# Kernel tuning notes

Measured on AMD Instinct MI355X. Metric: run time of the kernel, lower is better.

## Reference

```python
import jax, jax.numpy as jnp
import numpy as np

D1, D2, DK, NH = 1024, 1024, 1024, 1
B, S = 4, 2048


def setup_inputs() -> dict:
    key = jax.random.key(0)
    ks = jax.random.split(key, 12)
    scale1 = 1.0 / np.sqrt(D1)
    scale2 = 1.0 / np.sqrt(D2)
    scalek = 1.0 / np.sqrt(DK)
    return {
        "x": jax.random.normal(ks[0], (B, S, D1), dtype=jnp.float32),
        "y": jax.random.normal(ks[1], (B, S, D2), dtype=jnp.float32),
        "adj": jax.random.uniform(ks[2], (B, S, S), dtype=jnp.float32),
        "Wq": jax.random.uniform(ks[3], (D1, DK), jnp.float32, -scale1, scale1),
        "bq": jax.random.uniform(ks[4], (DK,), jnp.float32, -scale1, scale1),
        "Wk": jax.random.uniform(ks[5], (D2, DK), jnp.float32, -scale2, scale2),
        "bk": jax.random.uniform(ks[6], (DK,), jnp.float32, -scale2, scale2),
        "Wv": jax.random.uniform(ks[7], (D2, DK), jnp.float32, -scale2, scale2),
        "bv": jax.random.uniform(ks[8], (DK,), jnp.float32, -scale2, scale2),
        "Wo": jax.random.uniform(ks[9], (DK, D2), jnp.float32, -scalek, scalek),
        "bo": jax.random.uniform(ks[10], (D2,), jnp.float32, -scalek, scalek),
    }


def reference(x, y, adj, Wq, bq, Wk, bk, Wv, bv, Wo, bo):
    # Single-head (n_heads=1) cross-attention with additive adjacency bias.
    dk_head = DK // NH
    norm = 1.0 / np.sqrt(DK)
    Q = (x @ Wq + bq).reshape(NH, B, S, dk_head)   # [h,b,s,d]
    K = (y @ Wk + bk).reshape(NH, B, S, dk_head)
    V = (y @ Wv + bv).reshape(NH, B, S, dk_head)
    att = jnp.einsum('hbsd,hbtd->hbst', Q, K) * norm  # [h,b,s,t]
    att = jax.nn.softmax(att + adj, axis=-1)          # adj [b,s,t] broadcasts over h
    tmp = jnp.einsum('hbst,hbtd->hbsd', att, V).reshape(B, S, -1)  # [b,s,dk]
    out = (tmp @ Wo + bo).reshape(-1, S, D2)
    return out
```

## Files before the change

### kernel.cpp

```cpp
#include <hip/hip_runtime.h>
#include <stdint.h>

typedef unsigned short u16;
using bf16x8 = __attribute__((ext_vector_type(8))) short;
using f32x4  = __attribute__((ext_vector_type(4))) float;

#define NORM 0.03125f

enum { M_PROJ = 0, M_EXP = 1, M_PV = 2, M_OUT = 3 };

__device__ __forceinline__ u16 f2bf(float f) {
  uint32_t u = __float_as_uint(f);
  return (u16)((u + 0x7FFFu + ((u >> 16) & 1u)) >> 16);
}

__device__ __forceinline__ void gload_lds16(const void* g, void* lds) {
  __builtin_amdgcn_global_load_lds(
      (const __attribute__((address_space(1))) uint32_t*)g,
      (__attribute__((address_space(3))) uint32_t*)lds, 16, 0, 0);
}

__global__ void k_cvt(const float* __restrict__ in, u16* __restrict__ out, int n4) {
  int i = blockIdx.x * blockDim.x + threadIdx.x;
  if (i >= n4) return;
  float4 v = ((const float4*)in)[i];
  uint32_t lo = f2bf(v.x) | ((uint32_t)f2bf(v.y) << 16);
  uint32_t hi = f2bf(v.z) | ((uint32_t)f2bf(v.w) << 16);
  ((uint2*)out)[i] = make_uint2(lo, hi);
}

__global__ void k_tc(const float* __restrict__ W0, const float* __restrict__ W1,
                     const float* __restrict__ W2, const float* __restrict__ W3,
                     u16* __restrict__ dst) {
  __shared__ float t[64][65];
  const float* W = blockIdx.z == 0 ? W0 : blockIdx.z == 1 ? W1 : blockIdx.z == 2 ? W2 : W3;
  u16* WT = dst + (size_t)blockIdx.z * (1024 * 1024);
  int c0 = blockIdx.x * 64, r0 = blockIdx.y * 64;
  int c = threadIdx.x & 63, q = threadIdx.x >> 6;
  for (int r = q; r < 64; r += 4) t[r][c] = W[(size_t)(r0 + r) * 1024 + c0 + c];
  __syncthreads();
  for (int r = q; r < 64; r += 4) WT[(size_t)(c0 + r) * 1024 + r0 + c] = f2bf(t[c][r]);
}

struct GArgs {
  const u16* A; const u16* B; int lda, ldb; long long bstrideB; int K;
  const float* bias; const float* adj; float* dpart; const float* dpart_r;
  void* C; int ldc;
  const u16* A1; const u16* B1; const u16* B2;
  const float* bias1; const float* bias2; void* C1; void* C2;
};

template <int MODE>
__global__ __launch_bounds__(512, 2) void gemm3(GArgs g) {
  __shared__ __align__(16) u16 sm[73728];

  const int tid = threadIdx.x, lane = tid & 63, wid = tid >> 6;
  const int wm = wid >> 2, wn = wid & 3;
  const int m0 = blockIdx.x * 128;
  const int n0 = blockIdx.y * 256;
  const int b = m0 >> 11;

  const u16* A = g.A; const u16* B = g.B;
  const float* bias = g.bias; void* C = g.C;
  int zmode = 0;
  if constexpr (MODE == M_PROJ) {
    int z = blockIdx.z; zmode = z;
    if (z == 1) { A = g.A1; B = g.B1; bias = g.bias1; C = g.C1; }
    else if (z == 2) { A = g.A1; B = g.B2; bias = g.bias2; C = g.C2; }
  }
  const int lda = g.lda, ldb = g.ldb, K = g.K, NT = K >> 6;
  const u16* Bp = B + (size_t)b * g.bstrideB;

  f32x4 acc[4][4] = {};

  const int srow = tid >> 2;
  const int scb = (tid & 3) * 16;
  auto stageA = [&](int v, int kh, int bufb) {
    int csw = scb ^ ((srow & 8) << 2);
    gload_lds16(A + (size_t)(m0 + srow) * lda + v * 64 + kh * 32 + (csw >> 1),
                (void*)&sm[bufb + kh * 4096 + srow * 32 + (tid & 3) * 8]);
  };
  auto stageB = [&](int v, int kh, int bufb) {
#pragma unroll
    for (int j = 0; j < 2; ++j) {
      int row = j * 128 + srow;
      int csw = scb ^ ((row & 8) << 2);
      gload_lds16(Bp + (size_t)(n0 + row) * ldb + v * 64 + kh * 32 + (csw >> 1),
                  (void*)&sm[bufb + 8192 + kh * 8192 + row * 32 + (tid & 3) * 8]);
    }
  };

  stageA(0, 0, 0);     stageB(0, 0, 0);
  stageA(0, 1, 0);     stageB(0, 1, 0);
  stageA(1, 0, 24576); stageB(1, 0, 24576);
  stageA(1, 1, 24576); stageB(1, 1, 24576);

  const int cb = (lane >> 4) * 16;
  const int fr = lane & 15;
  int rd = 0;
  for (int u = 0; u < NT; ++u) {
    const int bufb = rd * 24576;
    const int stb = (rd == 0 ? 2 : rd - 1) * 24576;
    if (u + 1 < NT) asm volatile("s_waitcnt vmcnt(6)" ::: "memory");
    else            asm volatile("s_waitcnt vmcnt(0)" ::: "memory");
    __builtin_amdgcn_s_barrier();
#pragma unroll
    for (int kh = 0; kh < 2; ++kh) {
      bf16x8 af[4], bfr[4];
#pragma unroll
      for (int m = 0; m < 4; ++m) {
        int row = wm * 64 + m * 16 + fr;
        af[m] = *(const bf16x8*)__builtin_assume_aligned(
            &sm[bufb + kh * 4096 + row * 32 + ((cb ^ ((row & 8) << 2)) >> 1)], 16);
      }
#pragma unroll
      for (int n = 0; n < 4; ++n) {
        int row = wn * 64 + n * 16 + fr;
        bfr[n] = *(const bf16x8*)__builtin_assume_aligned(
            &sm[bufb + 8192 + kh * 8192 + row * 32 + ((cb ^ ((row & 8) << 2)) >> 1)], 16);
      }
      if (u + 2 < NT) {
        stageA(u + 2, kh, stb);
        stageB(u + 2, kh, stb);
      }
      __builtin_amdgcn_s_setprio(1);
#pragma unroll
      for (int m = 0; m < 4; ++m)
#pragma unroll
        for (int n = 0; n < 4; ++n)
          acc[m][n] = __builtin_amdgcn_mfma_f32_16x16x32_bf16(
              af[m], bfr[n], acc[m][n], 0, 0, 0);
      __builtin_amdgcn_s_setprio(0);
    }
    rd = (rd == 2) ? 0 : rd + 1;
  }

  const int lr = lane >> 4, lc = lane & 15;

  if constexpr (MODE == M_PROJ) {
    if (zmode < 2) {
      u16* Cc = (u16*)C;
#pragma unroll
      for (int m = 0; m < 4; ++m)
#pragma unroll
        for (int n = 0; n < 4; ++n) {
          int gcol = n0 + wn * 64 + n * 16 + lc;
          float bv = bias[gcol];
#pragma unroll
          for (int r = 0; r < 4; ++r) {
            int grow = m0 + wm * 64 + m * 16 + lr * 4 + r;
            Cc[(size_t)grow * g.ldc + gcol] = f2bf(acc[m][n][r] + bv);
          }
        }
    } else {
      u16* Cc = (u16*)C;
#pragma unroll
      for (int m = 0; m < 4; ++m) {
        int grow0 = m0 + wm * 64 + m * 16 + lr * 4;
        int t0 = grow0 & 2047;
#pragma unroll
        for (int n = 0; n < 4; ++n) {
          int gcol = n0 + wn * 64 + n * 16 + lc;
          float bv = bias[gcol];
          ushort4 pk = make_ushort4(f2bf(acc[m][n][0] + bv), f2bf(acc[m][n][1] + bv),
                                    f2bf(acc[m][n][2] + bv), f2bf(acc[m][n][3] + bv));
          *(ushort4*)&Cc[((size_t)b * 1024 + gcol) * 2048 + t0] = pk;
        }
      }
    }
  } else if constexpr (MODE == M_EXP) {
    u16* Cc = (u16*)C;
    float esum[4][4];
#pragma unroll
    for (int m = 0; m < 4; ++m)
#pragma unroll
      for (int r = 0; r < 4; ++r) esum[m][r] = 0.f;
#pragma unroll
    for (int m = 0; m < 4; ++m)
#pragma unroll
      for (int n = 0; n < 4; ++n) {
        int gcol = n0 + wn * 64 + n * 16 + lc;
#pragma unroll
        for (int r = 0; r < 4; ++r) {
          int grow = m0 + wm * 64 + m * 16 + lr * 4 + r;
          float z = acc[m][n][r] * NORM + g.adj[(size_t)grow * 2048 + gcol];
          float e = __expf(z);
          Cc[(size_t)grow * 2048 + gcol] = f2bf(e);
          esum[m][r] += e;
        }
      }
    int pidx = blockIdx.y * 4 + wn;
#pragma unroll
    for (int m = 0; m < 4; ++m)
#pragma unroll
      for (int r = 0; r < 4; ++r) {
        float s = esum[m][r];
        s += __shfl_xor(s, 1); s += __shfl_xor(s, 2);
        s += __shfl_xor(s, 4); s += __shfl_xor(s, 8);
        if (lc == 0)
          g.dpart[(size_t)pidx * 8192 + m0 + wm * 64 + m * 16 + lr * 4 + r] = s;
      }
  } else if constexpr (MODE == M_PV) {
    __shared__ float dinv[128];
    if (tid < 128) {
      float s = 0.f;
#pragma unroll
      for (int t = 0; t < 32; ++t) s += g.dpart_r[(size_t)t * 8192 + m0 + tid];
      dinv[tid] = 1.0f / s;
    }
    __syncthreads();
    u16* Cc = (u16*)C;
#pragma unroll
    for (int m = 0; m < 4; ++m)
#pragma unroll
      for (int n = 0; n < 4; ++n) {
        int gcol = n0 + wn * 64 + n * 16 + lc;
#pragma unroll
        for (int r = 0; r < 4; ++r) {
          int lrow = wm * 64 + m * 16 + lr * 4 + r;
          Cc[(size_t)(m0 + lrow) * g.ldc + gcol] = f2bf(acc[m][n][r] * dinv[lrow]);
        }
      }
  } else {
    float* Cc = (float*)C;
#pragma unroll
    for (int m = 0; m < 4; ++m)
#pragma unroll
      for (int n = 0; n < 4; ++n) {
        int gcol = n0 + wn * 64 + n * 16 + lc;
        float bv = bias[gcol];
#pragma unroll
        for (int r = 0; r < 4; ++r) {
          int grow = m0 + wm * 64 + m * 16 + lr * 4 + r;
          Cc[(size_t)grow * g.ldc + gcol] = acc[m][n][r] + bv;
        }
      }
  }
}

extern "C" void kernel_launch(void* const* d_in, const int* in_sizes, int n_in,
                              void* d_out, int out_size, void* d_ws, size_t ws_size,
                              hipStream_t stream) {
  const float* x   = (const float*)d_in[0];
  const float* y   = (const float*)d_in[1];
  const float* adj = (const float*)d_in[2];
  const float* Wq  = (const float*)d_in[3];
  const float* bq  = (const float*)d_in[4];
  const float* Wk  = (const float*)d_in[5];
  const float* bk  = (const float*)d_in[6];
  const float* Wv  = (const float*)d_in[7];
  const float* bv  = (const float*)d_in[8];
  const float* Wo  = (const float*)d_in[9];
  const float* bo  = (const float*)d_in[10];
  float* out = (float*)d_out;

  char* ws = (char*)d_ws;
  if (ws_size < 143654912ULL) return;
  u16* xb = (u16*)(ws);
  u16* yb = (u16*)(ws + 16777216);
  u16* WT = (u16*)(ws + 33554432);
  u16* Qb = (u16*)(ws + 41943040);
  u16* Kb = (u16*)(ws + 58720256);
  u16* Vt = (u16*)(ws + 75497472);
  u16* E  = (u16*)(ws + 92274688);
  float* dpart = (float*)(ws + 125829120);
  u16* tmpb = (u16*)(ws + 126877696);

  u16* WqT = WT;
  u16* WkT = WT + 1048576;
  u16* WvT = WT + 2097152;
  u16* WoT = WT + 3145728;

  k_cvt<<<8192, 256, 0, stream>>>(x, xb, 2097152);
  k_cvt<<<8192, 256, 0, stream>>>(y, yb, 2097152);
  k_tc<<<dim3(16, 16, 4), 256, 0, stream>>>(Wq, Wk, Wv, Wo, WT);

  GArgs ga;
  ga.A = xb; ga.B = WqT; ga.lda = 1024; ga.ldb = 1024; ga.bstrideB = 0; ga.K = 1024;
  ga.bias = bq; ga.adj = nullptr; ga.dpart = nullptr; ga.dpart_r = nullptr;
  ga.C = Qb; ga.ldc = 1024;
  ga.A1 = yb; ga.B1 = WkT; ga.B2 = WvT; ga.bias1 = bk; ga.bias2 = bv;
  ga.C1 = Kb; ga.C2 = Vt;
  gemm3<M_PROJ><<<dim3(64, 4, 3), 512, 0, stream>>>(ga);

  GArgs ge = {};
  ge.A = Qb; ge.B = Kb; ge.lda = 1024; ge.ldb = 1024; ge.bstrideB = 2097152LL; ge.K = 1024;
  ge.bias = nullptr; ge.adj = adj; ge.dpart = dpart; ge.dpart_r = nullptr;
  ge.C = E; ge.ldc = 2048;
  gemm3<M_EXP><<<dim3(64, 8), 512, 0, stream>>>(ge);

  GArgs gp = {};
  gp.A = E; gp.B = Vt; gp.lda = 2048; gp.ldb = 2048; gp.bstrideB = 2097152LL; gp.K = 2048;
  gp.bias = nullptr; gp.adj = nullptr; gp.dpart = nullptr; gp.dpart_r = dpart;
  gp.C = tmpb; gp.ldc = 1024;
  gemm3<M_PV><<<dim3(64, 4), 512, 0, stream>>>(gp);

  GArgs go = {};
  go.A = tmpb; go.B = WoT; go.lda = 1024; go.ldb = 1024; go.bstrideB = 0; go.K = 1024;
  go.bias = bo; go.adj = nullptr; go.dpart = nullptr; go.dpart_r = nullptr;
  go.C = out; go.ldc = 1024;
  gemm3<M_OUT><<<dim3(64, 4), 512, 0, stream>>>(go);
}
```

Measured before the change: 229.7 us.

## Hand-schedule GEMM main loop with inline-asm LDS reads and split barriers

Rewrites the GEMM main loop so LDS fragment loads use inline ds_read_b128 with immediate offsets from precomputed base addresses. Each k-step is split into two halves: the first half issues the A-stage global loads, the second issues the B-stage loads. Barriers, explicit lgkmcnt/vmcnt waits and sched_barrier fence each MFMA block. The aim is to cut address arithmetic and control how global-to-LDS copies overlap with MFMA, in exchange for extra barriers per iteration and fragile hand-managed wait counts.

```diff
diff --git a/kernel.cpp b/kernel.cpp
--- a/kernel.cpp
+++ b/kernel.cpp
@@ -19,6 +19,10 @@
       (const __attribute__((address_space(1))) uint32_t*)g,
       (__attribute__((address_space(3))) uint32_t*)lds, 16, 0, 0);
 }
+
+#define DSR(dst, base, off)                                        \
+  asm volatile("ds_read_b128 %0, %1 offset:" #off                  \
+               : "=v"(dst) : "v"(base))
 
 __global__ void k_cvt(const float* __restrict__ in, u16* __restrict__ out, int n4) {
   int i = blockIdx.x * blockDim.x + threadIdx.x;
@@ -94,46 +98,71 @@
   stageA(0, 1, 0);     stageB(0, 1, 0);
   stageA(1, 0, 24576); stageB(1, 0, 24576);
   stageA(1, 1, 24576); stageB(1, 1, 24576);
-
-  const int cb = (lane >> 4) * 16;
+  asm volatile("s_waitcnt vmcnt(6)" ::: "memory");
+  __builtin_amdgcn_s_barrier();
+
+  const uint32_t smu = (uint32_t)(uintptr_t)&sm[0];
   const int fr = lane & 15;
+  const int swz = ((lane >> 4) * 16) ^ ((fr & 8) << 2);
+  const uint32_t arow = (uint32_t)((wm * 64 + fr) * 64 + swz);
+  const uint32_t brow = (uint32_t)(16384 + (wn * 64 + fr) * 64 + swz);
+
+  bf16x8 a0, a1, a2, a3, b0, b1, b2, b3;
+
+#define MFMA16()                                                            \
+  __builtin_amdgcn_s_setprio(1);                                            \
+  acc[0][0] = __builtin_amdgcn_mfma_f32_16x16x32_bf16(a0, b0, acc[0][0], 0, 0, 0); \
+  acc[0][1] = __builtin_amdgcn_mfma_f32_16x16x32_bf16(a0, b1, acc[0][1], 0, 0, 0); \
+  acc[0][2] = __builtin_amdgcn_mfma_f32_16x16x32_bf16(a0, b2, acc[0][2], 0, 0, 0); \
+  acc[0][3] = __builtin_amdgcn_mfma_f32_16x16x32_bf16(a0, b3, acc[0][3], 0, 0, 0); \
+  acc[1][0] = __builtin_amdgcn_mfma_f32_16x16x32_bf16(a1, b0, acc[1][0], 0, 0, 0); \
+  acc[1][1] = __builtin_amdgcn_mfma_f32_16x16x32_bf16(a1, b1, acc[1][1], 0, 0, 0); \
+  acc[1][2] = __builtin_amdgcn_mfma_f32_16x16x32_bf16(a1, b2, acc[1][2], 0, 0, 0); \
+  acc[1][3] = __builtin_amdgcn_mfma_f32_16x16x32_bf16(a1, b3, acc[1][3], 0, 0, 0); \
+  acc[2][0] = __builtin_amdgcn_mfma_f32_16x16x32_bf16(a2, b0, acc[2][0], 0, 0, 0); \
+  acc[2][1] = __builtin_amdgcn_mfma_f32_16x16x32_bf16(a2, b1, acc[2][1], 0, 0, 0); \
+  acc[2][2] = __builtin_amdgcn_mfma_f32_16x16x32_bf16(a2, b2, acc[2][2], 0, 0, 0); \
+  acc[2][3] = __builtin_amdgcn_mfma_f32_16x16x32_bf16(a2, b3, acc[2][3], 0, 0, 0); \
+  acc[3][0] = __builtin_amdgcn_mfma_f32_16x16x32_bf16(a3, b0, acc[3][0], 0, 0, 0); \
+  acc[3][1] = __builtin_amdgcn_mfma_f32_16x16x32_bf16(a3, b1, acc[3][1], 0, 0, 0); \
+  acc[3][2] = __builtin_amdgcn_mfma_f32_16x16x32_bf16(a3, b2, acc[3][2], 0, 0, 0); \
+  acc[3][3] = __builtin_amdgcn_mfma_f32_16x16x32_bf16(a3, b3, acc[3][3], 0, 0, 0); \
+  __builtin_amdgcn_s_setprio(0);
+
   int rd = 0;
   for (int u = 0; u < NT; ++u) {
-    const int bufb = rd * 24576;
+    const uint32_t bb = smu + (uint32_t)rd * 49152u;
+    const uint32_t abase = bb + arow;
+    const uint32_t bbase = bb + brow;
     const int stb = (rd == 0 ? 2 : rd - 1) * 24576;
-    if (u + 1 < NT) asm volatile("s_waitcnt vmcnt(6)" ::: "memory");
-    else            asm volatile("s_waitcnt vmcnt(0)" ::: "memory");
+
+    DSR(a0, abase, 0);    DSR(a1, abase, 1024);
+    DSR(a2, abase, 2048); DSR(a3, abase, 3072);
+    DSR(b0, bbase, 0);    DSR(b1, bbase, 1024);
+    DSR(b2, bbase, 2048); DSR(b3, bbase, 3072);
+    if (u + 2 < NT) { stageA(u + 2, 0, stb); stageA(u + 2, 1, stb); }
     __builtin_amdgcn_s_barrier();
-#pragma unroll
-    for (int kh = 0; kh < 2; ++kh) {
-      bf16x8 af[4], bfr[4];
-#pragma unroll
-      for (int m = 0; m < 4; ++m) {
-        int row = wm * 64 + m * 16 + fr;
-        af[m] = *(const bf16x8*)__builtin_assume_aligned(
-            &sm[bufb + kh * 4096 + row * 32 + ((cb ^ ((row & 8) << 2)) >> 1)], 16);
-      }
-#pragma unroll
-      for (int n = 0; n < 4; ++n) {
-        int row = wn * 64 + n * 16 + fr;
-        bfr[n] = *(const bf16x8*)__builtin_assume_aligned(
-            &sm[bufb + 8192 + kh * 8192 + row * 32 + ((cb ^ ((row & 8) << 2)) >> 1)], 16);
-      }
-      if (u + 2 < NT) {
-        stageA(u + 2, kh, stb);
-        stageB(u + 2, kh, stb);
-      }
-      __builtin_amdgcn_s_setprio(1);
-#pragma unroll
-      for (int m = 0; m < 4; ++m)
-#pragma unroll
-        for (int n = 0; n < 4; ++n)
-          acc[m][n] = __builtin_amdgcn_mfma_f32_16x16x32_bf16(
-              af[m], bfr[n], acc[m][n], 0, 0, 0);
-      __builtin_amdgcn_s_setprio(0);
-    }
+    asm volatile("s_waitcnt lgkmcnt(0)" ::: "memory");
+    __builtin_amdgcn_sched_barrier(0);
+    MFMA16();
+    __builtin_amdgcn_s_barrier();
+
+    DSR(a0, abase, 8192);  DSR(a1, abase, 9216);
+    DSR(a2, abase, 10240); DSR(a3, abase, 11264);
+    DSR(b0, bbase, 16384); DSR(b1, bbase, 17408);
+    DSR(b2, bbase, 18432); DSR(b3, bbase, 19456);
+    if (u + 2 < NT) { stageB(u + 2, 0, stb); stageB(u + 2, 1, stb); }
+    __builtin_amdgcn_s_barrier();
+    asm volatile("s_waitcnt lgkmcnt(0)" ::: "memory");
+    __builtin_amdgcn_sched_barrier(0);
+    MFMA16();
+    if (u + 2 < NT)      asm volatile("s_waitcnt vmcnt(6)" ::: "memory");
+    else if (u + 1 < NT) asm volatile("s_waitcnt vmcnt(0)" ::: "memory");
+    __builtin_amdgcn_s_barrier();
+
     rd = (rd == 2) ? 0 : rd + 1;
   }
+#undef MFMA16
 
   const int lr = lane >> 4, lc = lane & 15;
 
```

Measured after the change: 226.0 us. Within noise of the previous version (-1.6%).

## Replace pipelined 128x256 GEMM with single-buffered 128x128 high-occupancy kernel

Applied to the files above, without the earlier changes.

Replaces the triple-buffered, async-prefetched 512-thread GEMM with a 256-thread kernel. The new kernel uses 128x128 tiles and a single LDS buffer, with a sync before and after each 64-wide K step. The goal is to raise occupancy (four blocks per CU) and run twice as many blocks, hiding memory latency through multiple resident blocks instead of explicit prefetch. Grids and the softmax partial-sum indexing are adjusted to match. The cost is that loads and MFMA work no longer overlap within a block, and the smaller N tile means the A operand is reused less.

```diff
diff --git a/kernel.cpp b/kernel.cpp
--- a/kernel.cpp
+++ b/kernel.cpp
@@ -51,13 +51,17 @@
 };
 
 template <int MODE>
-__global__ __launch_bounds__(512, 2) void gemm3(GArgs g) {
-  __shared__ __align__(16) u16 sm[73728];
-
-  const int tid = threadIdx.x, lane = tid & 63, wid = tid >> 6;
-  const int wm = wid >> 2, wn = wid & 3;
+__global__ __launch_bounds__(256, 4) void gemm_occ(GArgs g) {
+  __shared__ __align__(16) u16 As[128 * 64];
+  __shared__ __align__(16) u16 Bs[128 * 64];
+
+  const int tid = threadIdx.x;
+  const int lane = tid & 63;
+  const int wid = tid >> 6;
+  const int wr = wid >> 1, wc = wid & 1;
+
   const int m0 = blockIdx.x * 128;
-  const int n0 = blockIdx.y * 256;
+  const int n0 = blockIdx.y * 128;
   const int b = m0 >> 11;
 
   const u16* A = g.A; const u16* B = g.B;
@@ -68,74 +72,53 @@
     if (z == 1) { A = g.A1; B = g.B1; bias = g.bias1; C = g.C1; }
     else if (z == 2) { A = g.A1; B = g.B2; bias = g.bias2; C = g.C2; }
   }
-  const int lda = g.lda, ldb = g.ldb, K = g.K, NT = K >> 6;
+  const int lda = g.lda, ldb = g.ldb, K = g.K;
   const u16* Bp = B + (size_t)b * g.bstrideB;
 
   f32x4 acc[4][4] = {};
 
-  const int srow = tid >> 2;
-  const int scb = (tid & 3) * 16;
-  auto stageA = [&](int v, int kh, int bufb) {
-    int csw = scb ^ ((srow & 8) << 2);
-    gload_lds16(A + (size_t)(m0 + srow) * lda + v * 64 + kh * 32 + (csw >> 1),
-                (void*)&sm[bufb + kh * 4096 + srow * 32 + (tid & 3) * 8]);
-  };
-  auto stageB = [&](int v, int kh, int bufb) {
-#pragma unroll
-    for (int j = 0; j < 2; ++j) {
-      int row = j * 128 + srow;
-      int csw = scb ^ ((row & 8) << 2);
-      gload_lds16(Bp + (size_t)(n0 + row) * ldb + v * 64 + kh * 32 + (csw >> 1),
-                  (void*)&sm[bufb + 8192 + kh * 8192 + row * 32 + (tid & 3) * 8]);
-    }
-  };
-
-  stageA(0, 0, 0);     stageB(0, 0, 0);
-  stageA(0, 1, 0);     stageB(0, 1, 0);
-  stageA(1, 0, 24576); stageB(1, 0, 24576);
-  stageA(1, 1, 24576); stageB(1, 1, 24576);
-
-  const int cb = (lane >> 4) * 16;
+  const int ric = lane >> 3;
+  const int c8 = (lane & 7) * 8;
+
   const int fr = lane & 15;
-  int rd = 0;
-  for (int u = 0; u < NT; ++u) {
-    const int bufb = rd * 24576;
-    const int stb = (rd == 0 ? 2 : rd - 1) * 24576;
-    if (u + 1 < NT) asm volatile("s_waitcnt vmcnt(6)" ::: "memory");
-    else            asm volatile("s_waitcnt vmcnt(0)" ::: "memory");
-    __builtin_amdgcn_s_barrier();
-#pragma unroll
-    for (int kh = 0; kh < 2; ++kh) {
+  const int hi = lane >> 4;
+
+  for (int kt = 0; kt < K; kt += 64) {
+#pragma unroll
+    for (int c = 0; c < 4; ++c) {
+      int ch = wid * 4 + c;
+      int row = ch * 8 + ric;
+      int swc = c8 ^ ((row & 7) << 3);
+      gload_lds16(A + (size_t)(m0 + row) * lda + kt + swc, (void*)&As[ch * 512]);
+      gload_lds16(Bp + (size_t)(n0 + row) * ldb + kt + swc, (void*)&Bs[ch * 512]);
+    }
+    __syncthreads();
+#pragma unroll
+    for (int kk = 0; kk < 64; kk += 32) {
       bf16x8 af[4], bfr[4];
 #pragma unroll
       for (int m = 0; m < 4; ++m) {
-        int row = wm * 64 + m * 16 + fr;
+        int row = wr * 64 + m * 16 + fr;
         af[m] = *(const bf16x8*)__builtin_assume_aligned(
-            &sm[bufb + kh * 4096 + row * 32 + ((cb ^ ((row & 8) << 2)) >> 1)], 16);
-      }
-#pragma unroll
-      for (int n = 0; n < 4; ++n) {
-        int row = wn * 64 + n * 16 + fr;
+            &As[row * 64 + ((kk + hi * 8) ^ ((row & 7) << 3))], 16);
+      }
+#pragma unroll
+      for (int n = 0; n < 4; ++n) {
+        int row = wc * 64 + n * 16 + fr;
         bfr[n] = *(const bf16x8*)__builtin_assume_aligned(
-            &sm[bufb + 8192 + kh * 8192 + row * 32 + ((cb ^ ((row & 8) << 2)) >> 1)], 16);
-      }
-      if (u + 2 < NT) {
-        stageA(u + 2, kh, stb);
-        stageB(u + 2, kh, stb);
-      }
-      __builtin_amdgcn_s_setprio(1);
+            &Bs[row * 64 + ((kk + hi * 8) ^ ((row & 7) << 3))], 16);
+      }
 #pragma unroll
       for (int m = 0; m < 4; ++m)
 #pragma unroll
         for (int n = 0; n < 4; ++n)
-          acc[m][n] = __builtin_amdgcn_mfma_f32_16x16x32_bf16(
-              af[m], bfr[n], acc[m][n], 0, 0, 0);
-      __builtin_amdgcn_s_setprio(0);
-    }
-    rd = (rd == 2) ? 0 : rd + 1;
+          acc[m][n] = __builtin_amdgcn_mfma_f32_16x16x32_bf16(af[m], bfr[n], acc[m][n], 0, 0, 0);
+    }
+    __syncthreads();
   }
 
-  const int lr = lane >> 4, lc = lane & 15;
+  const int lr = lane >> 4;
+  const int lc = lane & 15;
 
   if constexpr (MODE == M_PROJ) {
     if (zmode < 2) {
@@ -144,11 +127,11 @@
       for (int m = 0; m < 4; ++m)
 #pragma unroll
         for (int n = 0; n < 4; ++n) {
-          int gcol = n0 + wn * 64 + n * 16 + lc;
+          int gcol = n0 + wc * 64 + n * 16 + lc;
           float bv = bias[gcol];
 #pragma unroll
           for (int r = 0; r < 4; ++r) {
-            int grow = m0 + wm * 64 + m * 16 + lr * 4 + r;
+            int grow = m0 + wr * 64 + m * 16 + lr * 4 + r;
             Cc[(size_t)grow * g.ldc + gcol] = f2bf(acc[m][n][r] + bv);
           }
         }
@@ -156,11 +139,11 @@
       u16* Cc = (u16*)C;
 #pragma unroll
       for (int m = 0; m < 4; ++m) {
-        int grow0 = m0 + wm * 64 + m * 16 + lr * 4;
+        int grow0 = m0 + wr * 64 + m * 16 + lr * 4;
         int t0 = grow0 & 2047;
 #pragma unroll
         for (int n = 0; n < 4; ++n) {
-          int gcol = n0 + wn * 64 + n * 16 + lc;
+          int gcol = n0 + wc * 64 + n * 16 + lc;
           float bv = bias[gcol];
           ushort4 pk = make_ushort4(f2bf(acc[m][n][0] + bv), f2bf(acc[m][n][1] + bv),
                                     f2bf(acc[m][n][2] + bv), f2bf(acc[m][n][3] + bv));
@@ -170,26 +153,22 @@
     }
   } else if constexpr (MODE == M_EXP) {
     u16* Cc = (u16*)C;
-    float esum[4][4];
-#pragma unroll
-    for (int m = 0; m < 4; ++m)
-#pragma unroll
-      for (int r = 0; r < 4; ++r) esum[m][r] = 0.f;
-#pragma unroll
-    for (int m = 0; m < 4; ++m)
-#pragma unroll
-      for (int n = 0; n < 4; ++n) {
-        int gcol = n0 + wn * 64 + n * 16 + lc;
+    float esum[4][4] = {};
+#pragma unroll
+    for (int m = 0; m < 4; ++m)
+#pragma unroll
+      for (int n = 0; n < 4; ++n) {
+        int gcol = n0 + wc * 64 + n * 16 + lc;
 #pragma unroll
         for (int r = 0; r < 4; ++r) {
-          int grow = m0 + wm * 64 + m * 16 + lr * 4 + r;
+          int grow = m0 + wr * 64 + m * 16 + lr * 4 + r;
           float z = acc[m][n][r] * NORM + g.adj[(size_t)grow * 2048 + gcol];
           float e = __expf(z);
           Cc[(size_t)grow * 2048 + gcol] = f2bf(e);
           esum[m][r] += e;
         }
       }
-    int pidx = blockIdx.y * 4 + wn;
+    int pidx = blockIdx.y * 2 + wc;
 #pragma unroll
     for (int m = 0; m < 4; ++m)
 #pragma unroll
@@ -198,7 +177,7 @@
         s += __shfl_xor(s, 1); s += __shfl_xor(s, 2);
         s += __shfl_xor(s, 4); s += __shfl_xor(s, 8);
         if (lc == 0)
-          g.dpart[(size_t)pidx * 8192 + m0 + wm * 64 + m * 16 + lr * 4 + r] = s;
+          g.dpart[(size_t)pidx * 8192 + (m0 + wr * 64 + m * 16 + lr * 4 + r)] = s;
       }
   } else if constexpr (MODE == M_PV) {
     __shared__ float dinv[128];
@@ -214,10 +193,10 @@
     for (int m = 0; m < 4; ++m)
 #pragma unroll
       for (int n = 0; n < 4; ++n) {
-        int gcol = n0 + wn * 64 + n * 16 + lc;
+        int gcol = n0 + wc * 64 + n * 16 + lc;
 #pragma unroll
         for (int r = 0; r < 4; ++r) {
-          int lrow = wm * 64 + m * 16 + lr * 4 + r;
+          int lrow = wr * 64 + m * 16 + lr * 4 + r;
           Cc[(size_t)(m0 + lrow) * g.ldc + gcol] = f2bf(acc[m][n][r] * dinv[lrow]);
         }
       }
@@ -227,11 +206,11 @@
     for (int m = 0; m < 4; ++m)
 #pragma unroll
       for (int n = 0; n < 4; ++n) {
-        int gcol = n0 + wn * 64 + n * 16 + lc;
+        int gcol = n0 + wc * 64 + n * 16 + lc;
         float bv = bias[gcol];
 #pragma unroll
         for (int r = 0; r < 4; ++r) {
-          int grow = m0 + wm * 64 + m * 16 + lr * 4 + r;
+          int grow = m0 + wr * 64 + m * 16 + lr * 4 + r;
           Cc[(size_t)grow * g.ldc + gcol] = acc[m][n][r] + bv;
         }
       }
@@ -281,23 +260,23 @@
   ga.C = Qb; ga.ldc = 1024;
   ga.A1 = yb; ga.B1 = WkT; ga.B2 = WvT; ga.bias1 = bk; ga.bias2 = bv;
   ga.C1 = Kb; ga.C2 = Vt;
-  gemm3<M_PROJ><<<dim3(64, 4, 3), 512, 0, stream>>>(ga);
+  gemm_occ<M_PROJ><<<dim3(64, 8, 3), 256, 0, stream>>>(ga);
 
   GArgs ge = {};
   ge.A = Qb; ge.B = Kb; ge.lda = 1024; ge.ldb = 1024; ge.bstrideB = 2097152LL; ge.K = 1024;
   ge.bias = nullptr; ge.adj = adj; ge.dpart = dpart; ge.dpart_r = nullptr;
   ge.C = E; ge.ldc = 2048;
-  gemm3<M_EXP><<<dim3(64, 8), 512, 0, stream>>>(ge);
+  gemm_occ<M_EXP><<<dim3(64, 16), 256, 0, stream>>>(ge);
 
   GArgs gp = {};
   gp.A = E; gp.B = Vt; gp.lda = 2048; gp.ldb = 2048; gp.bstrideB = 2097152LL; gp.K = 2048;
   gp.bias = nullptr; gp.adj = nullptr; gp.dpart = nullptr; gp.dpart_r = dpart;
   gp.C = tmpb; gp.ldc = 1024;
-  gemm3<M_PV><<<dim3(64, 4), 512, 0, stream>>>(gp);
+  gemm_occ<M_PV><<<dim3(64, 8), 256, 0, stream>>>(gp);
 
   GArgs go = {};
   go.A = tmpb; go.B = WoT; go.lda = 1024; go.ldb = 1024; go.bstrideB = 0; go.K = 1024;
   go.bias = bo; go.adj = nullptr; go.dpart = nullptr; go.dpart_r = nullptr;
   go.C = out; go.ldc = 1024;
-  gemm3<M_OUT><<<dim3(64, 4), 512, 0, stream>>>(go);
-}
+  gemm_occ<M_OUT><<<dim3(64, 8), 256, 0, stream>>>(go);
+}
```

Measured after the change: 219.0 us. 1.05x faster.
